# Performance work log

Hardware: AMD Instinct MI355X
Metric: run time of the kernel (lower is better)

## Reference

```python
import jax, jax.numpy as jnp
import numpy as np
from math import sqrt

B, NQ, SK, ISIZE, HSIZE, OSIZE, H = 4, 2048, 2048, 1024, 1024, 1024, 16
D = HSIZE // H  # attn_dim = 64
IEPS = 1e-32
NEG = -1e32

def setup_inputs() -> dict:
    key = jax.random.key(0)
    ks = jax.random.split(key, 9)
    scale = 1.0 / sqrt(ISIZE)
    return {
        "iQ": jax.random.normal(ks[0], (B, NQ, ISIZE), jnp.float32),
        "iK": jax.random.normal(ks[1], (B, SK, ISIZE), jnp.float32),
        "iV": jax.random.normal(ks[2], (B, SK, ISIZE), jnp.float32),
        "mask": jax.random.randint(ks[3], (B, NQ, SK), 0, 2).astype(bool),
        # torch nn.Linear weights: [out_features, in_features]
        "Wq": jax.random.normal(ks[4], (HSIZE, ISIZE), jnp.float32) * scale,
        "Wk": jax.random.normal(ks[5], (HSIZE, ISIZE), jnp.float32) * scale,
        "Wv": jax.random.normal(ks[6], (HSIZE, ISIZE), jnp.float32) * scale,
        "Wo": jax.random.normal(ks[7], (OSIZE, HSIZE), jnp.float32) * scale,
        "sn_bias": jnp.zeros((1,), jnp.float32),  # SparseNormer bias
    }

def reference(iQ, iK, iV, mask, Wq, Wk, Wv, Wo, sn_bias):
    b, nq, _ = iQ.shape
    sk = iK.shape[1]
    # projections, split into heads: [b, h, n, d]
    q = (iQ @ Wq.T).reshape(b, nq, H, D).transpose(0, 2, 1, 3)
    k = (iK @ Wk.T).reshape(b, sk, H, D).transpose(0, 2, 1, 3)
    v = (iV @ Wv.T).reshape(b, sk, H, D).transpose(0, 2, 1, 3)
    # scaled dot-product scores: [b, h, nq, sk]
    scores = jnp.einsum("bhqd,bhkd->bhqk", q, k) / sqrt(D)
    scores = jnp.where(mask[:, None, :, :], NEG, scores)
    # SparseNormer: relu(x + bias)^2 normalized along last dim
    t = jax.nn.relu(scores + sn_bias)
    t = t * t
    attn = t / (t.sum(-1, keepdims=True) + IEPS)
    o = jnp.einsum("bhqk,bhkd->bhqd", attn, v)
    o = o.transpose(0, 2, 1, 3).reshape(b, nq, HSIZE)
    return o @ Wo.T
```

## Files before the change

kernel.cpp:

```cpp
#include <hip/hip_runtime.h>
#include <stdint.h>

#define B_   4
#define NQ_  2048
#define SK_  2048
#define H_   16
#define HS_  1024
#define D_   64

typedef __attribute__((ext_vector_type(8))) short bf16x8;
typedef __attribute__((ext_vector_type(4))) float f32x4;
typedef __attribute__((ext_vector_type(8))) unsigned short u16x8;
typedef __attribute__((ext_vector_type(4))) int i32x4;

#define DEVI __device__ __forceinline__

DEVI unsigned short f2bf_hu(float f) {
  union { float f; unsigned int i; } x; x.f = f;
  return (unsigned short)((x.i + 0x8000u) >> 16);
}
DEVI unsigned int pack2(float a, float b) {
  union { float f; unsigned int i; } x, y; x.f = a; y.f = b;
  return __builtin_amdgcn_perm(y.i + 0x8000u, x.i + 0x8000u, 0x07060302u);
}
DEVI u16x8 cvt8(f32x4 lo, f32x4 hi) {
  union { u16x8 s; unsigned int w[4]; } r;
  r.w[0] = pack2(lo[0], lo[1]);
  r.w[1] = pack2(lo[2], lo[3]);
  r.w[2] = pack2(hi[0], hi[1]);
  r.w[3] = pack2(hi[2], hi[3]);
  return r.s;
}

template <bool ABF16, bool CF32>
__global__ __launch_bounds__(256)
void gemm_bt(const void* __restrict__ Ap, const float* __restrict__ W,
             void* __restrict__ Cp, int M, int N, int K) {
  __shared__ unsigned short As[128 * 40];
  __shared__ unsigned short Bs[128 * 40];
  const int t = threadIdx.x;
  const int w = t >> 6, l = t & 63;
  const int lm = l & 15, lg = l >> 4;
  const int bm = blockIdx.x * 128, bn = blockIdx.y * 128;
  const int wm = (w >> 1) * 64, wn = (w & 1) * 64;

  const int sr = t >> 2, sc = (t & 3) * 8;
  const float* Af = (const float*)Ap;
  const unsigned short* Ab = (const unsigned short*)Ap;
  const size_t ao0 = (size_t)(bm + sr) * K + sc;
  const size_t ao1 = (size_t)(bm + sr + 64) * K + sc;
  const size_t wo0 = (size_t)(bn + sr) * K + sc;
  const size_t wo1 = (size_t)(bn + sr + 64) * K + sc;

  auto loadA = [&](size_t off) -> u16x8 {
    if constexpr (ABF16) {
      return *(const u16x8*)(Ab + off);
    } else {
      f32x4 lo = *(const f32x4*)(Af + off);
      f32x4 hi = *(const f32x4*)(Af + off + 4);
      return cvt8(lo, hi);
    }
  };
  auto loadW = [&](size_t off) -> u16x8 {
    f32x4 lo = *(const f32x4*)(W + off);
    f32x4 hi = *(const f32x4*)(W + off + 4);
    return cvt8(lo, hi);
  };

  u16x8 pa0 = loadA(ao0), pa1 = loadA(ao1);
  u16x8 pb0 = loadW(wo0), pb1 = loadW(wo1);

  f32x4 acc[4][4] = {};

  for (int k0 = 0; k0 < K; k0 += 32) {
    *(u16x8*)&As[sr * 40 + sc]        = pa0;
    *(u16x8*)&As[(sr + 64) * 40 + sc] = pa1;
    *(u16x8*)&Bs[sr * 40 + sc]        = pb0;
    *(u16x8*)&Bs[(sr + 64) * 40 + sc] = pb1;
    __syncthreads();
    if (k0 + 32 < K) {
      pa0 = loadA(ao0 + k0 + 32);
      pa1 = loadA(ao1 + k0 + 32);
      pb0 = loadW(wo0 + k0 + 32);
      pb1 = loadW(wo1 + k0 + 32);
    }
    bf16x8 aF[4], bF[4];
#pragma unroll
    for (int i = 0; i < 4; i++)
      aF[i] = *(const bf16x8*)&As[(wm + i * 16 + lm) * 40 + lg * 8];
#pragma unroll
    for (int i = 0; i < 4; i++)
      bF[i] = *(const bf16x8*)&Bs[(wn + i * 16 + lm) * 40 + lg * 8];
#pragma unroll
    for (int i = 0; i < 4; i++)
#pragma unroll
      for (int j = 0; j < 4; j++)
        acc[i][j] = __builtin_amdgcn_mfma_f32_16x16x32_bf16(aF[i], bF[j], acc[i][j], 0, 0, 0);
    __syncthreads();
  }
#pragma unroll
  for (int i = 0; i < 4; i++)
#pragma unroll
    for (int j = 0; j < 4; j++) {
      const int row = bm + wm + i * 16 + lg * 4;
      const int col = bn + wn + j * 16 + lm;
#pragma unroll
      for (int r = 0; r < 4; r++) {
        if constexpr (CF32) {
          ((float*)Cp)[(size_t)(row + r) * N + col] = acc[i][j][r];
        } else {
          ((unsigned short*)Cp)[(size_t)(row + r) * N + col] = f2bf_hu(acc[i][j][r]);
        }
      }
    }
}

__global__ __launch_bounds__(256)
void attn_sn(const unsigned short* __restrict__ Qb,
             const unsigned short* __restrict__ Kb,
             const unsigned short* __restrict__ Vb,
             const int* __restrict__ mask,
             const float* __restrict__ snb,
             unsigned short* __restrict__ Ob) {
  __shared__ unsigned short Ks[64 * 72];
  __shared__ unsigned short Vt[64 * 72];
  __shared__ unsigned short Pq[128 * 72];
  __shared__ float denomS[128];

  const int h = blockIdx.x, qt = blockIdx.y, b = blockIdx.z;
  const int t = threadIdx.x, w = t >> 6, l = t & 63;
  const int lm = l & 15, lg = l >> 4;
  const int q0 = qt * 128;
  const int wk = (w >> 1) * 32;
  const int wn = (w & 1) * 64;
  const float bias = snb[0];

  bf16x8 bQ[4][2];
#pragma unroll
  for (int ni = 0; ni < 4; ni++)
#pragma unroll
    for (int kf = 0; kf < 2; kf++) {
      const int qq = q0 + wn + ni * 16 + lm;
      bQ[ni][kf] = *(const bf16x8*)&Qb[(size_t)(b * NQ_ + qq) * HS_ + h * D_ + kf * 32 + lg * 8];
    }

  const int kr = t >> 3, kc = (t & 7) * 8;
  const unsigned short* Kg = Kb + (size_t)(b * SK_) * HS_ + h * D_ + kc;
  const int va = t & 31;
  const int vc = (t >> 5) * 8;
  const unsigned short* Vg = Vb + (size_t)(b * SK_) * HS_ + h * D_ + vc;
  const int* mbase = mask + (size_t)b * NQ_ * SK_;

  f32x4 oacc[2][4] = {};
  float dpart[4] = {0.f, 0.f, 0.f, 0.f};

  u16x8 pk0 = *(const u16x8*)(Kg + (size_t)(kr) * HS_);
  u16x8 pk1 = *(const u16x8*)(Kg + (size_t)(32 + kr) * HS_);
  u16x8 pv0 = *(const u16x8*)(Vg + (size_t)(2 * va) * HS_);
  u16x8 pv1 = *(const u16x8*)(Vg + (size_t)(2 * va + 1) * HS_);

  for (int kt = 0; kt < SK_ / 64; kt++) {
    const int kk0 = kt * 64;
    *(u16x8*)&Ks[kr * 72 + kc]        = pk0;
    *(u16x8*)&Ks[(kr + 32) * 72 + kc] = pk1;
    {
      union { u16x8 s; unsigned int w4[4]; } a0, a1;
      a0.s = pv0; a1.s = pv1;
#pragma unroll
      for (int ww = 0; ww < 4; ww++) {
        unsigned int lo = __builtin_amdgcn_perm(a1.w4[ww], a0.w4[ww], 0x05040100u);
        unsigned int hi = __builtin_amdgcn_perm(a1.w4[ww], a0.w4[ww], 0x07060302u);
        *(unsigned int*)&Vt[(vc + 2 * ww) * 72 + 2 * va]     = lo;
        *(unsigned int*)&Vt[(vc + 2 * ww + 1) * 72 + 2 * va] = hi;
      }
    }
    __syncthreads();

    if (kt + 1 < SK_ / 64) {
      const int nk0 = kk0 + 64;
      pk0 = *(const u16x8*)(Kg + (size_t)(nk0 + kr) * HS_);
      pk1 = *(const u16x8*)(Kg + (size_t)(nk0 + 32 + kr) * HS_);
      pv0 = *(const u16x8*)(Vg + (size_t)(nk0 + 2 * va) * HS_);
      pv1 = *(const u16x8*)(Vg + (size_t)(nk0 + 2 * va + 1) * HS_);
    }
    i32x4 mq[4][2];
#pragma unroll
    for (int ni = 0; ni < 4; ni++) {
      const int* mrow = mbase + (size_t)(q0 + wn + ni * 16 + lm) * SK_ + kk0 + wk + lg * 4;
#pragma unroll
      for (int mi = 0; mi < 2; mi++) mq[ni][mi] = *(const i32x4*)(mrow + mi * 16);
    }

    bf16x8 aK[2][2];
#pragma unroll
    for (int mi = 0; mi < 2; mi++)
#pragma unroll
      for (int kf = 0; kf < 2; kf++)
        aK[mi][kf] = *(const bf16x8*)&Ks[(wk + mi * 16 + lm) * 72 + kf * 32 + lg * 8];
    f32x4 sf[2][4] = {};
#pragma unroll
    for (int mi = 0; mi < 2; mi++)
#pragma unroll
      for (int ni = 0; ni < 4; ni++) {
        sf[mi][ni] = __builtin_amdgcn_mfma_f32_16x16x32_bf16(aK[mi][0], bQ[ni][0], sf[mi][ni], 0, 0, 0);
        sf[mi][ni] = __builtin_amdgcn_mfma_f32_16x16x32_bf16(aK[mi][1], bQ[ni][1], sf[mi][ni], 0, 0, 0);
      }

#pragma unroll
    for (int ni = 0; ni < 4; ni++) {
      float dsum = 0.f;
#pragma unroll
      for (int mi = 0; mi < 2; mi++) {
        const i32x4 mw = mq[ni][mi];
        const f32x4 sv = sf[mi][ni];
        float x2[4];
#pragma unroll
        for (int r = 0; r < 4; r++) {
          float x = fmaxf(sv[r] * 0.125f + bias, 0.f);
          x = mw[r] ? 0.f : x;
          x2[r] = x * x;
          dsum += x2[r];
        }
        const unsigned long long pk =
            (unsigned long long)pack2(x2[0], x2[1]) |
            ((unsigned long long)pack2(x2[2], x2[3]) << 32);
        *(unsigned long long*)&Pq[(wn + ni * 16 + lm) * 72 + wk + mi * 16 + lg * 4] = pk;
      }
      dpart[ni] += dsum;
    }
    __syncthreads();

#pragma unroll
    for (int k2 = 0; k2 < 2; k2++) {
      bf16x8 aV[2], bP[4];
#pragma unroll
      for (int mi = 0; mi < 2; mi++)
        aV[mi] = *(const bf16x8*)&Vt[(wk + mi * 16 + lm) * 72 + k2 * 32 + lg * 8];
#pragma unroll
      for (int ni = 0; ni < 4; ni++)
        bP[ni] = *(const bf16x8*)&Pq[(wn + ni * 16 + lm) * 72 + k2 * 32 + lg * 8];
#pragma unroll
      for (int mi = 0; mi < 2; mi++)
#pragma unroll
        for (int ni = 0; ni < 4; ni++)
          oacc[mi][ni] = __builtin_amdgcn_mfma_f32_16x16x32_bf16(aV[mi], bP[ni], oacc[mi][ni], 0, 0, 0);
    }
    __syncthreads();
  }

#pragma unroll
  for (int ni = 0; ni < 4; ni++) {
    float v = dpart[ni];
    v += __shfl_xor(v, 16, 64);
    v += __shfl_xor(v, 32, 64);
    dpart[ni] = v;
  }
  if (((w >> 1) == 0) && (lg == 0)) {
#pragma unroll
    for (int ni = 0; ni < 4; ni++) denomS[wn + ni * 16 + lm] = dpart[ni];
  }
  __syncthreads();
  if (((w >> 1) == 1) && (lg == 0)) {
#pragma unroll
    for (int ni = 0; ni < 4; ni++) denomS[wn + ni * 16 + lm] += dpart[ni];
  }
  __syncthreads();

#pragma unroll
  for (int ni = 0; ni < 4; ni++) {
    const int ql = wn + ni * 16 + lm;
    const float inv = 1.0f / (denomS[ql] + 1e-32f);
#pragma unroll
    for (int mi = 0; mi < 2; mi++) {
      const int d0 = wk + mi * 16 + lg * 4;
      const f32x4 ov = oacc[mi][ni];
      const unsigned long long pk =
          (unsigned long long)pack2(ov[0] * inv, ov[1] * inv) |
          ((unsigned long long)pack2(ov[2] * inv, ov[3] * inv) << 32);
      *(unsigned long long*)&Pq[ql * 72 + d0] = pk;
    }
  }
  __syncthreads();
  const int qf = t >> 1;
  const int dg = (t & 1) * 32;
  unsigned short* orow = Ob + (size_t)(b * NQ_ + q0 + qf) * HS_ + h * D_ + dg;
#pragma unroll
  for (int j = 0; j < 4; j++) {
    u16x8 vv = *(const u16x8*)&Pq[qf * 72 + dg + j * 8];
    *(u16x8*)(orow + j * 8) = vv;
  }
}

extern "C" void kernel_launch(void* const* d_in, const int* in_sizes, int n_in,
                              void* d_out, int out_size, void* d_ws, size_t ws_size,
                              hipStream_t stream) {
  (void)in_sizes; (void)n_in; (void)out_size;
  const float* iQ  = (const float*)d_in[0];
  const float* iK  = (const float*)d_in[1];
  const float* iV  = (const float*)d_in[2];
  const int*   msk = (const int*)d_in[3];
  const float* Wq  = (const float*)d_in[4];
  const float* Wk  = (const float*)d_in[5];
  const float* Wv  = (const float*)d_in[6];
  const float* Wo  = (const float*)d_in[7];
  const float* snb = (const float*)d_in[8];
  float* out = (float*)d_out;

  const size_t TOK = (size_t)B_ * NQ_ * HS_;
  unsigned short *Qb, *Kb, *Vb, *Ob;
  if (ws_size >= 4 * TOK * sizeof(unsigned short)) {
    Qb = (unsigned short*)d_ws;
    Kb = Qb + TOK;
    Vb = Qb + 2 * TOK;
    Ob = Qb + 3 * TOK;
  } else {
    Qb = (unsigned short*)d_out;
    Kb = (unsigned short*)d_ws;
    Vb = Kb + TOK;
    Ob = Kb + 2 * TOK;
  }

  dim3 gg(64, 8, 1), bb(256, 1, 1);
  const int M = B_ * NQ_, N = HS_, K = HS_;
  hipLaunchKernelGGL((gemm_bt<false, false>), gg, bb, 0, stream, (const void*)iQ, Wq, (void*)Qb, M, N, K);
  hipLaunchKernelGGL((gemm_bt<false, false>), gg, bb, 0, stream, (const void*)iK, Wk, (void*)Kb, M, N, K);
  hipLaunchKernelGGL((gemm_bt<false, false>), gg, bb, 0, stream, (const void*)iV, Wv, (void*)Vb, M, N, K);
  hipLaunchKernelGGL(attn_sn, dim3(H_, NQ_ / 128, B_), bb, 0, stream,
                     Qb, Kb, Vb, msk, snb, Ob);
  hipLaunchKernelGGL((gemm_bt<true, true>), gg, bb, 0, stream, (const void*)Ob, Wo, (void*)out, M, N, K);
}
```

Before: 498.5 us.

## Pre-convert GEMM operands to bf16, use async LDS loads, bit-pack the mask

After: 485.6 us. -2.6%, faster.

```diff
diff --git a/kernel.cpp b/kernel.cpp
--- a/kernel.cpp
+++ b/kernel.cpp
@@ -30,6 +30,95 @@
   r.w[2] = pack2(hi[0], hi[1]);
   r.w[3] = pack2(hi[2], hi[3]);
   return r.s;
+}
+DEVI void async16(void* lds, const void* g) {
+  __builtin_amdgcn_global_load_lds(
+      (const __attribute__((address_space(1))) unsigned int*)g,
+      (__attribute__((address_space(3))) unsigned int*)lds, 16, 0, 0);
+}
+
+__global__ __launch_bounds__(256)
+void cvt_prep(const float* __restrict__ a, unsigned short* __restrict__ ab,
+              const float* __restrict__ wsrc, unsigned short* __restrict__ wdst,
+              int naBlocks) {
+  const int bi = blockIdx.x;
+  const float* s; unsigned short* d; size_t base;
+  if (bi < naBlocks) { s = a;    d = ab;   base = (size_t)bi * 2048; }
+  else               { s = wsrc; d = wdst; base = (size_t)(bi - naBlocks) * 2048; }
+  const size_t o = base + (size_t)threadIdx.x * 8;
+  f32x4 lo = *(const f32x4*)(s + o);
+  f32x4 hi = *(const f32x4*)(s + o + 4);
+  *(u16x8*)(d + o) = cvt8(lo, hi);
+}
+
+__global__ __launch_bounds__(256)
+void pack_mask(const int* __restrict__ m, unsigned long long* __restrict__ bits) {
+  const size_t tid = (size_t)blockIdx.x * 256 + threadIdx.x;
+  const unsigned long long bal = __ballot(m[tid] != 0);
+  if ((threadIdx.x & 63) == 0) bits[tid >> 6] = bal;
+}
+
+template <bool CF32>
+__global__ __launch_bounds__(256)
+void gemm_bb(const unsigned short* __restrict__ A, const unsigned short* __restrict__ Wb,
+             void* __restrict__ Cp, int M, int N, int K) {
+  __shared__ unsigned short As[128 * 32];
+  __shared__ unsigned short Bs[128 * 32];
+  const int t = threadIdx.x;
+  const int w = t >> 6, l = t & 63;
+  const int lm = l & 15, lg = l >> 4;
+  const int bm = blockIdx.x * 128, bn = blockIdx.y * 128;
+  const int wm = (w >> 1) * 64, wn = (w & 1) * 64;
+
+  const int sr = t >> 2;
+  const int sg = ((t & 3) ^ ((t >> 3) & 3)) * 8;
+  const unsigned short* Ag0 = A + (size_t)(bm + sr) * K + sg;
+  const unsigned short* Ag1 = A + (size_t)(bm + sr + 64) * K + sg;
+  const unsigned short* Wg0 = Wb + (size_t)(bn + sr) * K + sg;
+  const unsigned short* Wg1 = Wb + (size_t)(bn + sr + 64) * K + sg;
+  unsigned short* lA0 = &As[t * 8];
+  unsigned short* lA1 = &As[t * 8 + 2048];
+  unsigned short* lB0 = &Bs[t * 8];
+  unsigned short* lB1 = &Bs[t * 8 + 2048];
+
+  const int fx = (lm >> 1) & 3;
+  f32x4 acc[4][4] = {};
+
+  for (int k0 = 0; k0 < K; k0 += 32) {
+    async16(lA0, Ag0 + k0);
+    async16(lA1, Ag1 + k0);
+    async16(lB0, Wg0 + k0);
+    async16(lB1, Wg1 + k0);
+    __syncthreads();
+    bf16x8 aF[4], bF[4];
+#pragma unroll
+    for (int i = 0; i < 4; i++)
+      aF[i] = *(const bf16x8*)&As[(wm + i * 16 + lm) * 32 + ((lg ^ fx) * 8)];
+#pragma unroll
+    for (int i = 0; i < 4; i++)
+      bF[i] = *(const bf16x8*)&Bs[(wn + i * 16 + lm) * 32 + ((lg ^ fx) * 8)];
+#pragma unroll
+    for (int i = 0; i < 4; i++)
+#pragma unroll
+      for (int j = 0; j < 4; j++)
+        acc[i][j] = __builtin_amdgcn_mfma_f32_16x16x32_bf16(aF[i], bF[j], acc[i][j], 0, 0, 0);
+    __syncthreads();
+  }
+#pragma unroll
+  for (int i = 0; i < 4; i++)
+#pragma unroll
+    for (int j = 0; j < 4; j++) {
+      const int row = bm + wm + i * 16 + lg * 4;
+      const int col = bn + wn + j * 16 + lm;
+#pragma unroll
+      for (int r = 0; r < 4; r++) {
+        if constexpr (CF32) {
+          ((float*)Cp)[(size_t)(row + r) * N + col] = acc[i][j][r];
+        } else {
+          ((unsigned short*)Cp)[(size_t)(row + r) * N + col] = f2bf_hu(acc[i][j][r]);
+        }
+      }
+    }
 }
 
 template <bool ABF16, bool CF32>
@@ -43,7 +132,6 @@
   const int lm = l & 15, lg = l >> 4;
   const int bm = blockIdx.x * 128, bn = blockIdx.y * 128;
   const int wm = (w >> 1) * 64, wn = (w & 1) * 64;
-
   const int sr = t >> 2, sc = (t & 3) * 8;
   const float* Af = (const float*)Ap;
   const unsigned short* Ab = (const unsigned short*)Ap;
@@ -51,7 +139,6 @@
   const size_t ao1 = (size_t)(bm + sr + 64) * K + sc;
   const size_t wo0 = (size_t)(bn + sr) * K + sc;
   const size_t wo1 = (size_t)(bn + sr + 64) * K + sc;
-
   auto loadA = [&](size_t off) -> u16x8 {
     if constexpr (ABF16) {
       return *(const u16x8*)(Ab + off);
@@ -66,12 +153,9 @@
     f32x4 hi = *(const f32x4*)(W + off + 4);
     return cvt8(lo, hi);
   };
-
   u16x8 pa0 = loadA(ao0), pa1 = loadA(ao1);
   u16x8 pb0 = loadW(wo0), pb1 = loadW(wo1);
-
   f32x4 acc[4][4] = {};
-
   for (int k0 = 0; k0 < K; k0 += 32) {
     *(u16x8*)&As[sr * 40 + sc]        = pa0;
     *(u16x8*)&As[(sr + 64) * 40 + sc] = pa1;
@@ -115,11 +199,13 @@
     }
 }
 
+template <bool BITMASK>
 __global__ __launch_bounds__(256)
 void attn_sn(const unsigned short* __restrict__ Qb,
              const unsigned short* __restrict__ Kb,
              const unsigned short* __restrict__ Vb,
              const int* __restrict__ mask,
+             const unsigned int* __restrict__ bits,
              const float* __restrict__ snb,
              unsigned short* __restrict__ Ob) {
   __shared__ unsigned short Ks[64 * 72];
@@ -184,11 +270,18 @@
       pv1 = *(const u16x8*)(Vg + (size_t)(nk0 + 2 * va + 1) * HS_);
     }
     i32x4 mq[4][2];
-#pragma unroll
-    for (int ni = 0; ni < 4; ni++) {
-      const int* mrow = mbase + (size_t)(q0 + wn + ni * 16 + lm) * SK_ + kk0 + wk + lg * 4;
-#pragma unroll
-      for (int mi = 0; mi < 2; mi++) mq[ni][mi] = *(const i32x4*)(mrow + mi * 16);
+    unsigned int mb[4];
+    if constexpr (BITMASK) {
+#pragma unroll
+      for (int ni = 0; ni < 4; ni++)
+        mb[ni] = bits[(size_t)(b * NQ_ + q0 + wn + ni * 16 + lm) * 64 + kt * 2 + (wk >> 5)];
+    } else {
+#pragma unroll
+      for (int ni = 0; ni < 4; ni++) {
+        const int* mrow = mbase + (size_t)(q0 + wn + ni * 16 + lm) * SK_ + kk0 + wk + lg * 4;
+#pragma unroll
+        for (int mi = 0; mi < 2; mi++) mq[ni][mi] = *(const i32x4*)(mrow + mi * 16);
+      }
     }
 
     bf16x8 aK[2][2];
@@ -211,13 +304,16 @@
       float dsum = 0.f;
 #pragma unroll
       for (int mi = 0; mi < 2; mi++) {
-        const i32x4 mw = mq[ni][mi];
         const f32x4 sv = sf[mi][ni];
         float x2[4];
 #pragma unroll
         for (int r = 0; r < 4; r++) {
           float x = fmaxf(sv[r] * 0.125f + bias, 0.f);
-          x = mw[r] ? 0.f : x;
+          if constexpr (BITMASK) {
+            x = ((mb[ni] >> (mi * 16 + lg * 4 + r)) & 1u) ? 0.f : x;
+          } else {
+            x = mq[ni][mi][r] ? 0.f : x;
+          }
           x2[r] = x * x;
           dsum += x2[r];
         }
@@ -307,25 +403,55 @@
   float* out = (float*)d_out;
 
   const size_t TOK = (size_t)B_ * NQ_ * HS_;
-  unsigned short *Qb, *Kb, *Vb, *Ob;
-  if (ws_size >= 4 * TOK * sizeof(unsigned short)) {
-    Qb = (unsigned short*)d_ws;
-    Kb = Qb + TOK;
-    Vb = Qb + 2 * TOK;
-    Ob = Qb + 3 * TOK;
+  const size_t WE  = (size_t)HS_ * HS_;
+  const size_t BITS_B = (size_t)B_ * NQ_ * SK_ / 8;
+  const size_t NEED = (3 * TOK + WE) * 2 + BITS_B;
+
+  const dim3 gg(64, 8, 1), bb(256, 1, 1);
+  const dim3 ga(H_, NQ_ / 128, B_);
+  const int M = B_ * NQ_, N = HS_, K = HS_;
+
+  if (ws_size >= NEED) {
+    unsigned short* Kb = (unsigned short*)d_ws;
+    unsigned short* Vb = Kb + TOK;
+    unsigned short* Ob = Vb + TOK;
+    unsigned short* Wb = Ob + TOK;
+    unsigned int* bits = (unsigned int*)(Wb + WE);
+    unsigned short* out_us = (unsigned short*)d_out;
+    unsigned short* Qb  = out_us;
+    unsigned short* INb = out_us + TOK;
+
+    hipLaunchKernelGGL(cvt_prep, dim3(4608), bb, 0, stream, iQ, INb, Wq, Wb, 4096);
+    hipLaunchKernelGGL((gemm_bb<false>), gg, bb, 0, stream, INb, Wb, (void*)Qb, M, N, K);
+    hipLaunchKernelGGL(cvt_prep, dim3(4608), bb, 0, stream, iK, INb, Wk, Wb, 4096);
+    hipLaunchKernelGGL((gemm_bb<false>), gg, bb, 0, stream, INb, Wb, (void*)Kb, M, N, K);
+    hipLaunchKernelGGL(cvt_prep, dim3(4608), bb, 0, stream, iV, INb, Wv, Wb, 4096);
+    hipLaunchKernelGGL((gemm_bb<false>), gg, bb, 0, stream, INb, Wb, (void*)Vb, M, N, K);
+    hipLaunchKernelGGL(cvt_prep, dim3(512), bb, 0, stream,
+                       (const float*)nullptr, (unsigned short*)nullptr, Wo, Wb, 0);
+    hipLaunchKernelGGL(pack_mask, dim3(65536), bb, 0, stream,
+                       msk, (unsigned long long*)bits);
+    hipLaunchKernelGGL((attn_sn<true>), ga, bb, 0, stream,
+                       Qb, Kb, Vb, msk, bits, snb, Ob);
+    hipLaunchKernelGGL((gemm_bb<true>), gg, bb, 0, stream, Ob, Wb, (void*)out, M, N, K);
   } else {
-    Qb = (unsigned short*)d_out;
-    Kb = (unsigned short*)d_ws;
-    Vb = Kb + TOK;
-    Ob = Kb + 2 * TOK;
-  }
-
-  dim3 gg(64, 8, 1), bb(256, 1, 1);
-  const int M = B_ * NQ_, N = HS_, K = HS_;
-  hipLaunchKernelGGL((gemm_bt<false, false>), gg, bb, 0, stream, (const void*)iQ, Wq, (void*)Qb, M, N, K);
-  hipLaunchKernelGGL((gemm_bt<false, false>), gg, bb, 0, stream, (const void*)iK, Wk, (void*)Kb, M, N, K);
-  hipLaunchKernelGGL((gemm_bt<false, false>), gg, bb, 0, stream, (const void*)iV, Wv, (void*)Vb, M, N, K);
-  hipLaunchKernelGGL(attn_sn, dim3(H_, NQ_ / 128, B_), bb, 0, stream,
-                     Qb, Kb, Vb, msk, snb, Ob);
-  hipLaunchKernelGGL((gemm_bt<true, true>), gg, bb, 0, stream, (const void*)Ob, Wo, (void*)out, M, N, K);
-}
+    unsigned short *Qb, *Kb, *Vb, *Ob;
+    if (ws_size >= 4 * TOK * sizeof(unsigned short)) {
+      Qb = (unsigned short*)d_ws;
+      Kb = Qb + TOK;
+      Vb = Qb + 2 * TOK;
+      Ob = Qb + 3 * TOK;
+    } else {
+      Qb = (unsigned short*)d_out;
+      Kb = (unsigned short*)d_ws;
+      Vb = Kb + TOK;
+      Ob = Kb + 2 * TOK;
+    }
+    hipLaunchKernelGGL((gemm_bt<false, false>), gg, bb, 0, stream, (const void*)iQ, Wq, (void*)Qb, M, N, K);
+    hipLaunchKernelGGL((gemm_bt<false, false>), gg, bb, 0, stream, (const void*)iK, Wk, (void*)Kb, M, N, K);
+    hipLaunchKernelGGL((gemm_bt<false, false>), gg, bb, 0, stream, (const void*)iV, Wv, (void*)Vb, M, N, K);
+    hipLaunchKernelGGL((attn_sn<false>), ga, bb, 0, stream,
+                       Qb, Kb, Vb, msk, (const unsigned int*)nullptr, snb, Ob);
+    hipLaunchKernelGGL((gemm_bt<true, true>), gg, bb, 0, stream, (const void*)Ob, Wo, (void*)out, M, N, K);
+  }
+}
```
